# Kernel optimization log

Hardware: AMD Instinct MI355X
Metric: run time of the kernel (lower is better)

Reference implementation:

```python
import jax, jax.numpy as jnp
import numpy as np

N, C_IN, C_OUT, T, V = 32, 4, 64, 6, 512


def setup_inputs() -> dict:
    key = jax.random.key(0)
    ks = jax.random.split(key, 8)
    x = jax.random.normal(ks[0], (N, C_IN, T, V), dtype=jnp.float32)
    # A carries 7 (unused) adjacency channels + 1 binary mask channel
    A = jax.random.randint(ks[1], (N, 8, V, V), 0, 2, dtype=jnp.int32)
    conv_w = jax.random.normal(ks[2], (C_OUT, C_IN), dtype=jnp.float32) / np.sqrt(C_IN).astype(np.float32)
    conv_b = jax.random.normal(ks[3], (C_OUT,), dtype=jnp.float32) * 0.02
    l2_w = jax.random.normal(ks[4], (1, T), dtype=jnp.float32) / np.sqrt(T).astype(np.float32)
    l2_b = jax.random.normal(ks[5], (1,), dtype=jnp.float32) * 0.02
    l1_w = jax.random.normal(ks[6], (1, 2 * C_OUT), dtype=jnp.float32) / np.sqrt(2 * C_OUT).astype(np.float32)
    l1_b = jax.random.normal(ks[7], (1,), dtype=jnp.float32) * 0.02
    return {"x": x, "A": A, "conv_w": conv_w, "conv_b": conv_b,
            "l2_w": l2_w, "l2_b": l2_b, "l1_w": l1_w, "l1_b": l1_b}


def reference(x, A, conv_w, conv_b, l2_w, l2_b, l1_w, l1_b):
    c = conv_w.shape[0]
    # 1x1 conv over (t, v): pure channel mix
    xc = jnp.einsum('nctv,oc->notv', x, conv_w) + conv_b[None, :, None, None]  # (n, 64, t, v)
    # temporal squeeze via l2: Linear(6 -> 1) on last (t) axis
    x1 = jnp.einsum('nctv,t->nvc', xc, l2_w[0]) + l2_b[0]  # (n, v, 64)
    # GAT-style pairwise score: l1(cat(x1_i, x1_j)) decomposes into two rank-1 terms
    e_i = x1 @ l1_w[0, :c]   # (n, v)
    e_j = x1 @ l1_w[0, c:]   # (n, v)
    scores = e_i[:, :, None] + e_j[:, None, :] + l1_b[0]  # (n, v, v), [n,i,j]
    scores = jnp.where(scores >= 0, scores, 0.2 * scores)  # LeakyReLU(0.2)
    # mask channel: A[:,7]; mask.long()==0 -> -inf
    mask = A[:, 7]  # (n, v, v) int
    scores = jnp.where(mask == 0, -jnp.inf, scores)
    p = jax.nn.softmax(scores, axis=2)
    p = jnp.where(jnp.isnan(p), 0.0, p)  # fully-masked rows -> 0
    # aggregate: nctv,ndvw->nctw with d=1
    out = jnp.einsum('nctv,nvw->nctw', xc, p)
    return out, p[:, None]  # (n, 64, t, v), (n, 1, v, v)
```

## Files before the change

### kernel.cpp

```cpp
#include <hip/hip_runtime.h>
#include <math.h>

#define NB   32
#define CIN  4
#define COUT 64
#define TT   6
#define VV   512
#define P_OFF (NB*COUT*TT*VV)
#define SPLITS 8
#define CH   (VV/SPLITS)
#define NROW 24
#define E_FLOATS (2*NB*VV)

__global__ __launch_bounds__(256) void e_kernel(
    const float* __restrict__ x,
    const float* __restrict__ conv_w,
    const float* __restrict__ conv_b,
    const float* __restrict__ l2_w,
    const float* __restrict__ l2_b,
    const float* __restrict__ l1_w,
    float* __restrict__ e)
{
    __shared__ float W1[CIN], W2[CIN], cst[2];
    int tid = threadIdx.x;
    if (tid < CIN) {
        float w1 = 0.f, w2 = 0.f;
        for (int o = 0; o < COUT; ++o) {
            w1 += l1_w[o]        * conv_w[o*CIN + tid];
            w2 += l1_w[COUT + o] * conv_w[o*CIN + tid];
        }
        W1[tid] = w1; W2[tid] = w2;
    }
    if (tid == CIN) {
        float B1 = 0.f, B2 = 0.f, S1 = 0.f, S2 = 0.f;
        for (int o = 0; o < COUT; ++o) {
            B1 += l1_w[o]        * conv_b[o];
            B2 += l1_w[COUT + o] * conv_b[o];
            S1 += l1_w[o];
            S2 += l1_w[COUT + o];
        }
        float Ls = 0.f;
        for (int t = 0; t < TT; ++t) Ls += l2_w[t];
        cst[0] = Ls*B1 + l2_b[0]*S1;
        cst[1] = Ls*B2 + l2_b[0]*S2;
    }
    __syncthreads();

    int idx = blockIdx.x * 256 + tid;
    int n = idx >> 9, v = idx & (VV-1);
    float ei = cst[0], ej = cst[1];
    #pragma unroll
    for (int c = 0; c < CIN; ++c) {
        float wc1 = W1[c], wc2 = W2[c];
        #pragma unroll
        for (int t = 0; t < TT; ++t) {
            float xv = x[((n*CIN + c)*TT + t)*VV + v];
            float lw = l2_w[t];
            ei += lw*wc1*xv;
            ej += lw*wc2*xv;
        }
    }
    e[idx]         = ei;
    e[NB*VV + idx] = ej;
}

__global__ __launch_bounds__(512, 2) void fused_kernel(
    const float* __restrict__ x,
    const int*   __restrict__ A,
    const float* __restrict__ e,
    const float* __restrict__ l1_b,
    float*       __restrict__ p,
    float*       __restrict__ ypart)
{
    __shared__ float xst[CH][4][8];
    __shared__ float ps[2][16][VV];

    int s = blockIdx.x;
    int n = blockIdx.y;
    int tid = threadIdx.x;
    int lane = tid & 63;
    int q = tid >> 6;
    int rg = q >> 1;
    int wh = q & 1;

    for (int l = tid; l < NROW*CH; l += 512) {
        int r = l >> 6, i = l & 63;
        xst[i][r/6][r%6] = x[((size_t)n*NROW + r)*VV + s*CH + i];
    }

    float l1b_val = l1_b[0];
    float4 ej0 = *(const float4*)(e + NB*VV + n*VV + lane*8);
    float4 ej1 = *(const float4*)(e + NB*VV + n*VV + lane*8 + 4);
    float ejv[8] = {ej0.x, ej0.y, ej0.z, ej0.w, ej1.x, ej1.y, ej1.z, ej1.w};

    const int* mbase = A + (size_t)(n*8 + 7)*VV*VV;

    float acc[6][4];
    #pragma unroll
    for (int rr = 0; rr < 6; ++rr)
        #pragma unroll
        for (int k = 0; k < 4; ++k) acc[rr][k] = 0.f;
    float a24[4] = {0.f, 0.f, 0.f, 0.f};

    int iA0 = s*CH + q*2;
    int4 mA0, mA1, mB0, mB1;
    float bA, bB;
    {
        const int* mrA = mbase + (size_t)iA0*VV + lane*8;
        mA0 = *(const int4*)mrA;       mA1 = *(const int4*)(mrA + 4);
        mB0 = *(const int4*)(mrA+VV);  mB1 = *(const int4*)(mrA + VV + 4);
        bA = e[n*VV + iA0]; bB = e[n*VV + iA0 + 1];
    }

    for (int sub = 0; sub < 4; ++sub) {
        int i_gA = s*CH + sub*16 + q*2;

        int4 cA0 = mA0, cA1 = mA1, cB0 = mB0, cB1 = mB1;
        float biasA = bA + l1b_val, biasB = bB + l1b_val;

        if (sub < 3) {
            const int* mrA = mbase + (size_t)(i_gA + 16)*VV + lane*8;
            mA0 = *(const int4*)mrA;       mA1 = *(const int4*)(mrA + 4);
            mB0 = *(const int4*)(mrA+VV);  mB1 = *(const int4*)(mrA + VV + 4);
            bA = e[n*VV + i_gA + 16]; bB = e[n*VV + i_gA + 17];
        }

        float svA[8], svB[8];
        int mkA[8] = {cA0.x,cA0.y,cA0.z,cA0.w, cA1.x,cA1.y,cA1.z,cA1.w};
        int mkB[8] = {cB0.x,cB0.y,cB0.z,cB0.w, cB1.x,cB1.y,cB1.z,cB1.w};
        #pragma unroll
        for (int m2 = 0; m2 < 8; ++m2) {
            float tA = biasA + ejv[m2]; tA = (tA >= 0.f) ? tA : 0.2f*tA;
            svA[m2] = (mkA[m2] == 0) ? -INFINITY : tA;
            float tB = biasB + ejv[m2]; tB = (tB >= 0.f) ? tB : 0.2f*tB;
            svB[m2] = (mkB[m2] == 0) ? -INFINITY : tB;
        }
        float mA = svA[0], mB = svB[0];
        #pragma unroll
        for (int m2 = 1; m2 < 8; ++m2) {
            mA = fmaxf(mA, svA[m2]); mB = fmaxf(mB, svB[m2]);
        }
        #pragma unroll
        for (int off = 32; off; off >>= 1) {
            mA = fmaxf(mA, __shfl_xor(mA, off));
            mB = fmaxf(mB, __shfl_xor(mB, off));
        }
        float sumA = 0.f, sumB = 0.f;
        if (mA > -INFINITY) {
            #pragma unroll
            for (int m2 = 0; m2 < 8; ++m2) { svA[m2] = __expf(svA[m2]-mA); sumA += svA[m2]; }
        } else {
            #pragma unroll
            for (int m2 = 0; m2 < 8; ++m2) svA[m2] = 0.f;
        }
        if (mB > -INFINITY) {
            #pragma unroll
            for (int m2 = 0; m2 < 8; ++m2) { svB[m2] = __expf(svB[m2]-mB); sumB += svB[m2]; }
        } else {
            #pragma unroll
            for (int m2 = 0; m2 < 8; ++m2) svB[m2] = 0.f;
        }
        #pragma unroll
        for (int off = 32; off; off >>= 1) {
            sumA += __shfl_xor(sumA, off);
            sumB += __shfl_xor(sumB, off);
        }
        float invA = (sumA > 0.f) ? 1.f/sumA : 0.f;
        float invB = (sumB > 0.f) ? 1.f/sumB : 0.f;

        float4 pA03 = {svA[0]*invA, svA[1]*invA, svA[2]*invA, svA[3]*invA};
        float4 pA47 = {svA[4]*invA, svA[5]*invA, svA[6]*invA, svA[7]*invA};
        float4 pB03 = {svB[0]*invB, svB[1]*invB, svB[2]*invB, svB[3]*invB};
        float4 pB47 = {svB[4]*invB, svB[5]*invB, svB[6]*invB, svB[7]*invB};

        float* prA = p + ((size_t)(n*VV + i_gA))*VV + lane*8;
        *(float4*)prA            = pA03;
        *(float4*)(prA + 4)      = pA47;
        *(float4*)(prA + VV)     = pB03;
        *(float4*)(prA + VV + 4) = pB47;

        float* pd = &ps[sub & 1][q*2][lane*8];
        *(float4*)pd          = pA03;
        *(float4*)(pd + 4)    = pA47;
        *(float4*)(pd + VV)   = pB03;
        *(float4*)(pd + VV+4) = pB47;

        __syncthreads();

        const float (*psb)[VV] = ps[sub & 1];
        #pragma unroll
        for (int i = 0; i < 16; ++i) {
            float4 pv = *(const float4*)&psb[i][wh*256 + lane*4];
            float4 xa = *(const float4*)&xst[sub*16 + i][rg][0];
            float2 xb = *(const float2*)&xst[sub*16 + i][rg][4];
            float xr[6] = {xa.x, xa.y, xa.z, xa.w, xb.x, xb.y};
            float pvk[4] = {pv.x, pv.y, pv.z, pv.w};
            #pragma unroll
            for (int rr = 0; rr < 6; ++rr)
                #pragma unroll
                for (int k = 0; k < 4; ++k)
                    acc[rr][k] = fmaf(xr[rr], pvk[k], acc[rr][k]);
            if (rg == 0) {
                #pragma unroll
                for (int k = 0; k < 4; ++k) a24[k] += pvk[k];
            }
        }
    }

    float* yo = ypart + (size_t)(s*NB + n)*25*VV + wh*256 + lane*4;
    #pragma unroll
    for (int rr = 0; rr < 6; ++rr) {
        float4 st = {acc[rr][0], acc[rr][1], acc[rr][2], acc[rr][3]};
        *(float4*)(yo + (size_t)(rg*6 + rr)*VV) = st;
    }
    if (rg == 0) {
        float4 st = {a24[0], a24[1], a24[2], a24[3]};
        *(float4*)(yo + (size_t)24*VV) = st;
    }
}

__global__ __launch_bounds__(256) void expand_kernel(
    const float* __restrict__ ypart,
    const float* __restrict__ conv_w,
    const float* __restrict__ conv_b,
    float*       __restrict__ out)
{
    __shared__ float ysm[25][64];
    __shared__ float wsm[COUT*CIN];
    __shared__ float bsm[COUT];

    int wc = blockIdx.x;
    int n  = blockIdx.y;
    int tid = threadIdx.x;

    if (tid < COUT*CIN) wsm[tid] = conv_w[tid];
    if (tid < COUT)     bsm[tid] = conv_b[tid];

    for (int l4 = tid; l4 < 400; l4 += 256) {
        int r = l4 >> 4, w4 = l4 & 15;
        float4 a = {0.f, 0.f, 0.f, 0.f};
        #pragma unroll
        for (int s = 0; s < SPLITS; ++s) {
            float4 v = *(const float4*)(ypart +
                ((size_t)(s*NB + n)*25 + r)*VV + wc*64 + w4*4);
            a.x += v.x; a.y += v.y; a.z += v.z; a.w += v.w;
        }
        *(float4*)&ysm[r][w4*4] = a;
    }
    __syncthreads();

    int w  = tid & 63;
    int og = tid >> 6;

    float y[25];
    #pragma unroll
    for (int r = 0; r < 25; ++r) y[r] = ysm[r][w];

    #pragma unroll
    for (int oo = 0; oo < 16; ++oo) {
        int o = og*16 + oo;
        float wb[CIN];
        #pragma unroll
        for (int c = 0; c < CIN; ++c) wb[c] = wsm[o*CIN + c];
        float bo = bsm[o];
        #pragma unroll
        for (int t = 0; t < TT; ++t) {
            float val = bo * y[24];
            #pragma unroll
            for (int c = 0; c < CIN; ++c) val = fmaf(wb[c], y[c*TT + t], val);
            out[((size_t)(n*COUT + o)*TT + t)*VV + wc*64 + w] = val;
        }
    }
}

extern "C" void kernel_launch(void* const* d_in, const int* in_sizes, int n_in,
                              void* d_out, int out_size, void* d_ws, size_t ws_size,
                              hipStream_t stream)
{
    const float* x      = (const float*)d_in[0];
    const int*   A      = (const int*)  d_in[1];
    const float* conv_w = (const float*)d_in[2];
    const float* conv_b = (const float*)d_in[3];
    const float* l2_w   = (const float*)d_in[4];
    const float* l2_b   = (const float*)d_in[5];
    const float* l1_w   = (const float*)d_in[6];
    const float* l1_b   = (const float*)d_in[7];

    float* out = (float*)d_out;
    float* pP  = out + P_OFF;
    float* e   = (float*)d_ws;
    float* yp  = e + E_FLOATS;

    e_kernel<<<NB*VV/256, 256, 0, stream>>>(x, conv_w, conv_b, l2_w, l2_b, l1_w, e);

    dim3 gf(SPLITS, NB);
    fused_kernel<<<gf, 512, 0, stream>>>(x, A, e, l1_b, pP, yp);

    dim3 ge(8, NB);
    expand_kernel<<<ge, 256, 0, stream>>>(yp, conv_w, conv_b, out);
}
```

Baseline: 37.96 us.

## Stage softmax probabilities in LDS as bf16 and remap aggregation work

Stores the attention probability tile in shared memory as packed bf16 pairs instead of fp32, halving LDS footprint and read traffic in the aggregation loop. Each wave now covers 3 x-rows across all 512 columns (8 columns per lane) instead of 6 rows over half the columns, with the x staging layout changed to match. All four mask-row groups are loaded into registers up front rather than software-pipelined one step ahead. The bf16 rounding lowers precision of the aggregated output, and holding 16 int4 mask registers raises register pressure.

```diff
diff --git a/kernel.cpp b/kernel.cpp
--- a/kernel.cpp
+++ b/kernel.cpp
@@ -1,4 +1,5 @@
 #include <hip/hip_runtime.h>
+#include <hip/hip_bf16.h>
 #include <math.h>
 
 #define NB   32
@@ -11,6 +12,13 @@
 #define CH   (VV/SPLITS)
 #define NROW 24
 #define E_FLOATS (2*NB*VV)
+
+__device__ inline unsigned int pack2(float a, float b) {
+    __hip_bfloat162 h = __float22bfloat162_rn(make_float2(a, b));
+    return *reinterpret_cast<unsigned int*>(&h);
+}
+__device__ inline float blo(unsigned int u) { return __uint_as_float(u << 16); }
+__device__ inline float bhi(unsigned int u) { return __uint_as_float(u & 0xffff0000u); }
 
 __global__ __launch_bounds__(256) void e_kernel(
     const float* __restrict__ x,
@@ -72,20 +80,33 @@
     float*       __restrict__ p,
     float*       __restrict__ ypart)
 {
-    __shared__ float xst[CH][4][8];
-    __shared__ float ps[2][16][VV];
+    __shared__ float xst[CH][8][4];
+    __shared__ unsigned int ps[2][16][VV/2];
 
     int s = blockIdx.x;
     int n = blockIdx.y;
     int tid = threadIdx.x;
     int lane = tid & 63;
     int q = tid >> 6;
-    int rg = q >> 1;
-    int wh = q & 1;
 
     for (int l = tid; l < NROW*CH; l += 512) {
         int r = l >> 6, i = l & 63;
-        xst[i][r/6][r%6] = x[((size_t)n*NROW + r)*VV + s*CH + i];
+        xst[i][r/3][r%3] = x[((size_t)n*NROW + r)*VV + s*CH + i];
+    }
+
+    const int* mbase = A + (size_t)(n*8 + 7)*VV*VV;
+    int4 mreg[16];
+    float br[8];
+    #pragma unroll
+    for (int sub = 0; sub < 4; ++sub) {
+        int i0 = s*CH + sub*16 + q*2;
+        const int* mr = mbase + (size_t)i0*VV + lane*8;
+        mreg[sub*4+0] = *(const int4*)mr;
+        mreg[sub*4+1] = *(const int4*)(mr + 4);
+        mreg[sub*4+2] = *(const int4*)(mr + VV);
+        mreg[sub*4+3] = *(const int4*)(mr + VV + 4);
+        br[sub*2]   = e[n*VV + i0];
+        br[sub*2+1] = e[n*VV + i0 + 1];
     }
 
     float l1b_val = l1_b[0];
@@ -93,37 +114,20 @@
     float4 ej1 = *(const float4*)(e + NB*VV + n*VV + lane*8 + 4);
     float ejv[8] = {ej0.x, ej0.y, ej0.z, ej0.w, ej1.x, ej1.y, ej1.z, ej1.w};
 
-    const int* mbase = A + (size_t)(n*8 + 7)*VV*VV;
-
-    float acc[6][4];
-    #pragma unroll
-    for (int rr = 0; rr < 6; ++rr)
-        #pragma unroll
-        for (int k = 0; k < 4; ++k) acc[rr][k] = 0.f;
-    float a24[4] = {0.f, 0.f, 0.f, 0.f};
-
-    int iA0 = s*CH + q*2;
-    int4 mA0, mA1, mB0, mB1;
-    float bA, bB;
-    {
-        const int* mrA = mbase + (size_t)iA0*VV + lane*8;
-        mA0 = *(const int4*)mrA;       mA1 = *(const int4*)(mrA + 4);
-        mB0 = *(const int4*)(mrA+VV);  mB1 = *(const int4*)(mrA + VV + 4);
-        bA = e[n*VV + iA0]; bB = e[n*VV + iA0 + 1];
-    }
+    float acc[3][8];
+    #pragma unroll
+    for (int rr = 0; rr < 3; ++rr)
+        #pragma unroll
+        for (int m2 = 0; m2 < 8; ++m2) acc[rr][m2] = 0.f;
+    float a24[8] = {0.f,0.f,0.f,0.f,0.f,0.f,0.f,0.f};
+
 
     for (int sub = 0; sub < 4; ++sub) {
         int i_gA = s*CH + sub*16 + q*2;
 
-        int4 cA0 = mA0, cA1 = mA1, cB0 = mB0, cB1 = mB1;
-        float biasA = bA + l1b_val, biasB = bB + l1b_val;
-
-        if (sub < 3) {
-            const int* mrA = mbase + (size_t)(i_gA + 16)*VV + lane*8;
-            mA0 = *(const int4*)mrA;       mA1 = *(const int4*)(mrA + 4);
-            mB0 = *(const int4*)(mrA+VV);  mB1 = *(const int4*)(mrA + VV + 4);
-            bA = e[n*VV + i_gA + 16]; bB = e[n*VV + i_gA + 17];
-        }
+        int4 cA0 = mreg[sub*4+0], cA1 = mreg[sub*4+1];
+        int4 cB0 = mreg[sub*4+2], cB1 = mreg[sub*4+3];
+        float biasA = br[sub*2] + l1b_val, biasB = br[sub*2+1] + l1b_val;
 
         float svA[8], svB[8];
         int mkA[8] = {cA0.x,cA0.y,cA0.z,cA0.w, cA1.x,cA1.y,cA1.z,cA1.w};
@@ -168,54 +172,60 @@
         float invA = (sumA > 0.f) ? 1.f/sumA : 0.f;
         float invB = (sumB > 0.f) ? 1.f/sumB : 0.f;
 
-        float4 pA03 = {svA[0]*invA, svA[1]*invA, svA[2]*invA, svA[3]*invA};
-        float4 pA47 = {svA[4]*invA, svA[5]*invA, svA[6]*invA, svA[7]*invA};
-        float4 pB03 = {svB[0]*invB, svB[1]*invB, svB[2]*invB, svB[3]*invB};
-        float4 pB47 = {svB[4]*invB, svB[5]*invB, svB[6]*invB, svB[7]*invB};
+        float pA[8], pB[8];
+        #pragma unroll
+        for (int m2 = 0; m2 < 8; ++m2) { pA[m2] = svA[m2]*invA; pB[m2] = svB[m2]*invB; }
 
         float* prA = p + ((size_t)(n*VV + i_gA))*VV + lane*8;
+        float4 pA03 = {pA[0],pA[1],pA[2],pA[3]}, pA47 = {pA[4],pA[5],pA[6],pA[7]};
+        float4 pB03 = {pB[0],pB[1],pB[2],pB[3]}, pB47 = {pB[4],pB[5],pB[6],pB[7]};
         *(float4*)prA            = pA03;
         *(float4*)(prA + 4)      = pA47;
         *(float4*)(prA + VV)     = pB03;
         *(float4*)(prA + VV + 4) = pB47;
 
-        float* pd = &ps[sub & 1][q*2][lane*8];
-        *(float4*)pd          = pA03;
-        *(float4*)(pd + 4)    = pA47;
-        *(float4*)(pd + VV)   = pB03;
-        *(float4*)(pd + VV+4) = pB47;
+        uint4 ua = {pack2(pA[0],pA[1]), pack2(pA[2],pA[3]),
+                    pack2(pA[4],pA[5]), pack2(pA[6],pA[7])};
+        uint4 ub = {pack2(pB[0],pB[1]), pack2(pB[2],pB[3]),
+                    pack2(pB[4],pB[5]), pack2(pB[6],pB[7])};
+        *(uint4*)&ps[sub & 1][q*2    ][lane*4] = ua;
+        *(uint4*)&ps[sub & 1][q*2 + 1][lane*4] = ub;
 
         __syncthreads();
 
-        const float (*psb)[VV] = ps[sub & 1];
         #pragma unroll
         for (int i = 0; i < 16; ++i) {
-            float4 pv = *(const float4*)&psb[i][wh*256 + lane*4];
-            float4 xa = *(const float4*)&xst[sub*16 + i][rg][0];
-            float2 xb = *(const float2*)&xst[sub*16 + i][rg][4];
-            float xr[6] = {xa.x, xa.y, xa.z, xa.w, xb.x, xb.y};
-            float pvk[4] = {pv.x, pv.y, pv.z, pv.w};
-            #pragma unroll
-            for (int rr = 0; rr < 6; ++rr)
+            uint4 pu = *(const uint4*)&ps[sub & 1][i][lane*4];
+            float4 xq = *(const float4*)&xst[sub*16 + i][q][0];
+            float pv[8] = {blo(pu.x), bhi(pu.x), blo(pu.y), bhi(pu.y),
+                           blo(pu.z), bhi(pu.z), blo(pu.w), bhi(pu.w)};
+            #pragma unroll
+            for (int m2 = 0; m2 < 8; ++m2) {
+                acc[0][m2] = fmaf(xq.x, pv[m2], acc[0][m2]);
+                acc[1][m2] = fmaf(xq.y, pv[m2], acc[1][m2]);
+                acc[2][m2] = fmaf(xq.z, pv[m2], acc[2][m2]);
+            }
+            if (q == 0) {
                 #pragma unroll
-                for (int k = 0; k < 4; ++k)
-                    acc[rr][k] = fmaf(xr[rr], pvk[k], acc[rr][k]);
-            if (rg == 0) {
-                #pragma unroll
-                for (int k = 0; k < 4; ++k) a24[k] += pvk[k];
+                for (int m2 = 0; m2 < 8; ++m2) a24[m2] += pv[m2];
             }
         }
     }
 
-    float* yo = ypart + (size_t)(s*NB + n)*25*VV + wh*256 + lane*4;
-    #pragma unroll
-    for (int rr = 0; rr < 6; ++rr) {
-        float4 st = {acc[rr][0], acc[rr][1], acc[rr][2], acc[rr][3]};
-        *(float4*)(yo + (size_t)(rg*6 + rr)*VV) = st;
-    }
-    if (rg == 0) {
-        float4 st = {a24[0], a24[1], a24[2], a24[3]};
-        *(float4*)(yo + (size_t)24*VV) = st;
+    float* yo = ypart + (size_t)(s*NB + n)*25*VV + lane*8;
+    #pragma unroll
+    for (int rr = 0; rr < 3; ++rr) {
+        int row = q*3 + rr;
+        float4 s0 = {acc[rr][0], acc[rr][1], acc[rr][2], acc[rr][3]};
+        float4 s1 = {acc[rr][4], acc[rr][5], acc[rr][6], acc[rr][7]};
+        *(float4*)(yo + (size_t)row*VV)     = s0;
+        *(float4*)(yo + (size_t)row*VV + 4) = s1;
+    }
+    if (q == 0) {
+        float4 s0 = {a24[0], a24[1], a24[2], a24[3]};
+        float4 s1 = {a24[4], a24[5], a24[6], a24[7]};
+        *(float4*)(yo + (size_t)24*VV)     = s0;
+        *(float4*)(yo + (size_t)24*VV + 4) = s1;
     }
 }
 
```

Measured after the change: 50.73 us. +33.7%, slower.

## Compute attention aggregation with bf16 MFMA instead of scalar FMAs

Applied to the files above, without the earlier changes.

Replaces the per-thread fp32 FMA aggregation of softmax weights against the x tile with bf16 MFMA 16x16x32 instructions. Probabilities are packed into bf16 pairs in shared memory, and x gets an extra all-ones row so the row-sum falls out of the same matmul. Syncs drop from one per sub-block to two per pair, and launch bounds allow more blocks per CU. The cost is bf16 rounding of both p and x in the aggregated output, which may exceed fp32 tolerance.

```diff
diff --git a/kernel.cpp b/kernel.cpp
--- a/kernel.cpp
+++ b/kernel.cpp
@@ -1,4 +1,5 @@
 #include <hip/hip_runtime.h>
+#include <hip/hip_bf16.h>
 #include <math.h>
 
 #define NB   32
@@ -11,6 +12,15 @@
 #define CH   (VV/SPLITS)
 #define NROW 24
 #define E_FLOATS (2*NB*VV)
+#define PKW  516
+
+typedef __attribute__((ext_vector_type(8))) short bf16x8;
+typedef __attribute__((ext_vector_type(4))) float f32x4;
+
+__device__ inline unsigned int pack2(float a, float b) {
+    __hip_bfloat162 h = __float22bfloat162_rn(make_float2(a, b));
+    return *reinterpret_cast<unsigned int*>(&h);
+}
 
 __global__ __launch_bounds__(256) void e_kernel(
     const float* __restrict__ x,
@@ -64,7 +74,7 @@
     e[NB*VV + idx] = ej;
 }
 
-__global__ __launch_bounds__(512, 2) void fused_kernel(
+__global__ __launch_bounds__(512, 4) void fused_kernel(
     const float* __restrict__ x,
     const int*   __restrict__ A,
     const float* __restrict__ e,
@@ -72,20 +82,22 @@
     float*       __restrict__ p,
     float*       __restrict__ ypart)
 {
-    __shared__ float xst[CH][4][8];
-    __shared__ float ps[2][16][VV];
+    __shared__ float xst[CH][33];
+    __shared__ unsigned int pk[16][PKW];
 
     int s = blockIdx.x;
     int n = blockIdx.y;
     int tid = threadIdx.x;
     int lane = tid & 63;
     int q = tid >> 6;
-    int rg = q >> 1;
-    int wh = q & 1;
-
-    for (int l = tid; l < NROW*CH; l += 512) {
-        int r = l >> 6, i = l & 63;
-        xst[i][r/6][r%6] = x[((size_t)n*NROW + r)*VV + s*CH + i];
+
+    for (int idx = tid; idx < CH*33; idx += 512) {
+        int r = idx >> 6;
+        int i = idx & 63;
+        float v = 0.f;
+        if (r < NROW)       v = x[((size_t)n*NROW + r)*VV + s*CH + i];
+        else if (r == NROW) v = 1.f;
+        xst[i][r] = v;
     }
 
     float l1b_val = l1_b[0];
@@ -95,21 +107,22 @@
 
     const int* mbase = A + (size_t)(n*8 + 7)*VV*VV;
 
-    float acc[6][4];
-    #pragma unroll
-    for (int rr = 0; rr < 6; ++rr)
-        #pragma unroll
-        for (int k = 0; k < 4; ++k) acc[rr][k] = 0.f;
-    float a24[4] = {0.f, 0.f, 0.f, 0.f};
-
-    int iA0 = s*CH + q*2;
+    f32x4 acc[2][4];
+    #pragma unroll
+    for (int mt = 0; mt < 2; ++mt)
+        #pragma unroll
+        for (int t = 0; t < 4; ++t) acc[mt][t] = (f32x4){0.f, 0.f, 0.f, 0.f};
+
+    bf16x8 afr[2][2];
+
     int4 mA0, mA1, mB0, mB1;
     float bA, bB;
     {
-        const int* mrA = mbase + (size_t)iA0*VV + lane*8;
-        mA0 = *(const int4*)mrA;       mA1 = *(const int4*)(mrA + 4);
-        mB0 = *(const int4*)(mrA+VV);  mB1 = *(const int4*)(mrA + VV + 4);
-        bA = e[n*VV + iA0]; bB = e[n*VV + iA0 + 1];
+        int i0 = s*CH + q*2;
+        const int* mr = mbase + (size_t)i0*VV + lane*8;
+        mA0 = *(const int4*)mr;       mA1 = *(const int4*)(mr + 4);
+        mB0 = *(const int4*)(mr+VV);  mB1 = *(const int4*)(mr + VV + 4);
+        bA = e[n*VV + i0]; bB = e[n*VV + i0 + 1];
     }
 
     for (int sub = 0; sub < 4; ++sub) {
@@ -119,9 +132,9 @@
         float biasA = bA + l1b_val, biasB = bB + l1b_val;
 
         if (sub < 3) {
-            const int* mrA = mbase + (size_t)(i_gA + 16)*VV + lane*8;
-            mA0 = *(const int4*)mrA;       mA1 = *(const int4*)(mrA + 4);
-            mB0 = *(const int4*)(mrA+VV);  mB1 = *(const int4*)(mrA + VV + 4);
+            const int* mr = mbase + (size_t)(i_gA + 16)*VV + lane*8;
+            mA0 = *(const int4*)mr;       mA1 = *(const int4*)(mr + 4);
+            mB0 = *(const int4*)(mr+VV);  mB1 = *(const int4*)(mr + VV + 4);
             bA = e[n*VV + i_gA + 16]; bB = e[n*VV + i_gA + 17];
         }
 
@@ -167,56 +180,73 @@
         }
         float invA = (sumA > 0.f) ? 1.f/sumA : 0.f;
         float invB = (sumB > 0.f) ? 1.f/sumB : 0.f;
-
-        float4 pA03 = {svA[0]*invA, svA[1]*invA, svA[2]*invA, svA[3]*invA};
-        float4 pA47 = {svA[4]*invA, svA[5]*invA, svA[6]*invA, svA[7]*invA};
-        float4 pB03 = {svB[0]*invB, svB[1]*invB, svB[2]*invB, svB[3]*invB};
-        float4 pB47 = {svB[4]*invB, svB[5]*invB, svB[6]*invB, svB[7]*invB};
+        #pragma unroll
+        for (int m2 = 0; m2 < 8; ++m2) { svA[m2] *= invA; svB[m2] *= invB; }
 
         float* prA = p + ((size_t)(n*VV + i_gA))*VV + lane*8;
+        float4 pA03 = {svA[0],svA[1],svA[2],svA[3]}, pA47 = {svA[4],svA[5],svA[6],svA[7]};
+        float4 pB03 = {svB[0],svB[1],svB[2],svB[3]}, pB47 = {svB[4],svB[5],svB[6],svB[7]};
         *(float4*)prA            = pA03;
         *(float4*)(prA + 4)      = pA47;
         *(float4*)(prA + VV)     = pB03;
         *(float4*)(prA + VV + 4) = pB47;
 
-        float* pd = &ps[sub & 1][q*2][lane*8];
-        *(float4*)pd          = pA03;
-        *(float4*)(pd + 4)    = pA47;
-        *(float4*)(pd + VV)   = pB03;
-        *(float4*)(pd + VV+4) = pB47;
-
-        __syncthreads();
-
-        const float (*psb)[VV] = ps[sub & 1];
-        #pragma unroll
-        for (int i = 0; i < 16; ++i) {
-            float4 pv = *(const float4*)&psb[i][wh*256 + lane*4];
-            float4 xa = *(const float4*)&xst[sub*16 + i][rg][0];
-            float2 xb = *(const float2*)&xst[sub*16 + i][rg][4];
-            float xr[6] = {xa.x, xa.y, xa.z, xa.w, xb.x, xb.y};
-            float pvk[4] = {pv.x, pv.y, pv.z, pv.w};
-            #pragma unroll
-            for (int rr = 0; rr < 6; ++rr)
+        {
+            int pr = (sub & 1)*8 + q;
+            uint4 u0 = {pack2(svA[0],svB[0]), pack2(svA[1],svB[1]),
+                        pack2(svA[2],svB[2]), pack2(svA[3],svB[3])};
+            uint4 u1 = {pack2(svA[4],svB[4]), pack2(svA[5],svB[5]),
+                        pack2(svA[6],svB[6]), pack2(svA[7],svB[7])};
+            *(uint4*)&pk[pr][lane*8]     = u0;
+            *(uint4*)&pk[pr][lane*8 + 4] = u1;
+        }
+
+        if (sub & 1) {
+            __syncthreads();
+
+            if (sub == 1) {
                 #pragma unroll
-                for (int k = 0; k < 4; ++k)
-                    acc[rr][k] = fmaf(xr[rr], pvk[k], acc[rr][k]);
-            if (rg == 0) {
+                for (int g = 0; g < 2; ++g)
+                    #pragma unroll
+                    for (int mt = 0; mt < 2; ++mt) {
+                        int r  = mt*16 + (lane & 15);
+                        int kb = g*32 + (lane >> 4)*8;
+                        union { unsigned int u[4]; bf16x8 v; } ua;
+                        #pragma unroll
+                        for (int t = 0; t < 4; ++t)
+                            ua.u[t] = pack2(xst[kb + 2*t][r], xst[kb + 2*t + 1][r]);
+                        afr[g][mt] = ua.v;
+                    }
+            }
+
+            int g = sub >> 1;
+            #pragma unroll
+            for (int t = 0; t < 4; ++t) {
+                int ncol = (q*4 + t)*16 + (lane & 15);
+                union { unsigned int u[4]; bf16x8 v; } ub;
                 #pragma unroll
-                for (int k = 0; k < 4; ++k) a24[k] += pvk[k];
+                for (int jj = 0; jj < 4; ++jj)
+                    ub.u[jj] = pk[(lane >> 4)*4 + jj][ncol];
+                acc[0][t] = __builtin_amdgcn_mfma_f32_16x16x32_bf16(afr[g][0], ub.v, acc[0][t], 0, 0, 0);
+                acc[1][t] = __builtin_amdgcn_mfma_f32_16x16x32_bf16(afr[g][1], ub.v, acc[1][t], 0, 0, 0);
             }
-        }
-    }
-
-    float* yo = ypart + (size_t)(s*NB + n)*25*VV + wh*256 + lane*4;
-    #pragma unroll
-    for (int rr = 0; rr < 6; ++rr) {
-        float4 st = {acc[rr][0], acc[rr][1], acc[rr][2], acc[rr][3]};
-        *(float4*)(yo + (size_t)(rg*6 + rr)*VV) = st;
-    }
-    if (rg == 0) {
-        float4 st = {a24[0], a24[1], a24[2], a24[3]};
-        *(float4*)(yo + (size_t)24*VV) = st;
-    }
+            if (sub == 1) __syncthreads();
+        }
+    }
+
+    float* yo = ypart + (size_t)(s*NB + n)*25*VV;
+    #pragma unroll
+    for (int mt = 0; mt < 2; ++mt)
+        #pragma unroll
+        for (int t = 0; t < 4; ++t) {
+            int ncol = (q*4 + t)*16 + (lane & 15);
+            #pragma unroll
+            for (int reg = 0; reg < 4; ++reg) {
+                int row = mt*16 + (lane >> 4)*4 + reg;
+                if (row < 25)
+                    yo[(size_t)row*VV + ncol] = acc[mt][t][reg];
+            }
+        }
 }
 
 __global__ __launch_bounds__(256) void expand_kernel(
```

Measured after the change: 34.62 us. -8.8%, faster.
